# Kernel tuning notes

Hardware: AMD Instinct MI355X
Metric: run time of the kernel (lower is better)

The kernel has to match this reference:

```python
import jax, jax.numpy as jnp
import numpy as np

B, N, C, H = 4, 2048, 1024, 16
HD = C // H  # head dim = 64


def setup_inputs() -> dict:
    key = jax.random.key(0)
    k1, k2, k3, k4 = jax.random.split(key, 4)
    x = jax.random.normal(k1, (B, N, C), dtype=jnp.float32)
    # nn.Linear(C, 3C, bias=False): weight [3C, C], y = x @ W.T
    w_qkv = jax.random.normal(k2, (3 * C, C), dtype=jnp.float32) * (C ** -0.5)
    # nn.Linear(C, C) with bias
    w_out = jax.random.normal(k3, (C, C), dtype=jnp.float32) * (C ** -0.5)
    b_out = jax.random.normal(k4, (C,), dtype=jnp.float32) * 0.01
    return {"x": x, "w_qkv": w_qkv, "w_out": w_out, "b_out": b_out}


def reference(x, w_qkv, w_out, b_out):
    scale = HD ** -0.5
    qkv = jnp.einsum('bnc,dc->bnd', x, w_qkv)  # [B, N, 3C]
    q, k, v = jnp.split(qkv, 3, axis=-1)
    # rearrange 'b n (h c) -> b h n c'
    def heads(t):
        return t.reshape(B, N, H, HD).transpose(0, 2, 1, 3)
    q, k, v = heads(q) * scale, heads(k), heads(v)
    scores = jnp.einsum('bhnc,bhmc->bhnm', q, k)  # [B, H, N, N]
    attn = jax.nn.softmax(scores, axis=-1)
    v_hat = jnp.einsum('bhnm,bhmc->bhnc', attn, v)
    out = v_hat.transpose(0, 2, 1, 3).reshape(B, N, C)  # 'b h n c -> b n (h c)'
    return jnp.einsum('bnc,dc->bnd', out, w_out) + b_out
```

## Files before the change

kernel.cpp:

```cpp
#include <hip/hip_runtime.h>

typedef unsigned short ushort_t;
typedef __attribute__((ext_vector_type(8))) short short8;
typedef __attribute__((ext_vector_type(4))) float f32x4;
typedef __attribute__((ext_vector_type(16))) float f32x16;
typedef __attribute__((ext_vector_type(4))) float float4v;
typedef __attribute__((ext_vector_type(4))) unsigned short ushortx4;
typedef __attribute__((ext_vector_type(4))) unsigned int uint4v;

#define AS1 __attribute__((address_space(1)))
#define AS3 __attribute__((address_space(3)))

#define B_ 4
#define N_ 2048
#define C_ 1024
#define H_ 16
#define HD_ 64
#define M_TOT 8192
#define N3_ 3072

#define QSCALE 0.18033688011112042f

__device__ __forceinline__ unsigned short f2bf(float f) {
    unsigned int u = __float_as_uint(f);
    u += 0x7fffu + ((u >> 16) & 1u);
    return (unsigned short)(u >> 16);
}

__global__ __launch_bounds__(256) void cast_f32_bf16(const float* __restrict__ in,
                                                     ushort_t* __restrict__ out, int n4) {
    int i = blockIdx.x * blockDim.x + threadIdx.x;
    int stride = gridDim.x * blockDim.x;
    for (; i < n4; i += stride) {
        float4v v = ((const float4v*)in)[i];
        ushortx4 o;
        o[0] = f2bf(v[0]); o[1] = f2bf(v[1]); o[2] = f2bf(v[2]); o[3] = f2bf(v[3]);
        ((ushortx4*)out)[i] = o;
    }
}


template <int EPI>
__global__ __launch_bounds__(256) void gemm_bt(const ushort_t* __restrict__ A,
                                               const ushort_t* __restrict__ Bw,
                                               ushort_t* __restrict__ o0,
                                               ushort_t* __restrict__ o1,
                                               ushort_t* __restrict__ o2,
                                               float* __restrict__ outf,
                                               const float* __restrict__ bias, int K) {
    __shared__ ushort_t As[2][128 * 32];
    __shared__ ushort_t Bs[2][128 * 32];
    const int tid = threadIdx.x;
    const int lane = tid & 63;
    const int wid = tid >> 6;
    const int l15 = lane & 15, lg = lane >> 4;
    const int wr = wid >> 1, wc = wid & 1;
    const int m0 = blockIdx.y * 128, n0 = blockIdx.x * 128;

    f32x4 acc[4][4] = {};

    auto stage = [&](int buf, int k0) {
        int row = tid >> 2;
        int ko = (tid & 3) * 8;
        const ushort_t* a0 = A + (size_t)(m0 + row) * K + k0 + ko;
        const ushort_t* b0 = Bw + (size_t)(n0 + row) * K + k0 + ko;
        char* la = (char*)(&As[buf][0]) + (tid & 192) * 16;
        char* lb = (char*)(&Bs[buf][0]) + (tid & 192) * 16;
        __builtin_amdgcn_global_load_lds((const AS1 void*)a0, (AS3 void*)la, 16, 0, 0);
        __builtin_amdgcn_global_load_lds((const AS1 void*)(a0 + (size_t)64 * K),
                                         (AS3 void*)(la + 4096), 16, 0, 0);
        __builtin_amdgcn_global_load_lds((const AS1 void*)b0, (AS3 void*)lb, 16, 0, 0);
        __builtin_amdgcn_global_load_lds((const AS1 void*)(b0 + (size_t)64 * K),
                                         (AS3 void*)(lb + 4096), 16, 0, 0);
    };

    stage(0, 0);
    __syncthreads();
    const int NKI = K >> 5;
    for (int kt = 0; kt < NKI; ++kt) {
        const int cur = kt & 1;
        if (kt + 1 < NKI) stage(cur ^ 1, (kt + 1) << 5);
        short8 af[4], bf[4];
#pragma unroll
        for (int mi = 0; mi < 4; ++mi)
            af[mi] = *(const short8*)(&As[cur][(wr * 64 + mi * 16 + l15) * 32 + lg * 8]);
#pragma unroll
        for (int ni = 0; ni < 4; ++ni)
            bf[ni] = *(const short8*)(&Bs[cur][(wc * 64 + ni * 16 + l15) * 32 + lg * 8]);
#pragma unroll
        for (int mi = 0; mi < 4; ++mi)
#pragma unroll
            for (int ni = 0; ni < 4; ++ni)
                acc[mi][ni] = __builtin_amdgcn_mfma_f32_16x16x32_bf16(af[mi], bf[ni],
                                                                      acc[mi][ni], 0, 0, 0);
        __syncthreads();
    }

    if (EPI == 0) {
        const int sel = blockIdx.x >> 3;
        const int cb = (blockIdx.x & 7) * 128 + wc * 64;
#pragma unroll
        for (int mi = 0; mi < 4; ++mi) {
            const int r0 = m0 + wr * 64 + mi * 16 + lg * 4;
            const int b = r0 >> 11, n = r0 & 2047;
            const int blk = n >> 5, nlo = n & 31;
#pragma unroll
            for (int ni = 0; ni < 4; ++ni) {
                const int c = cb + ni * 16 + l15;
                const int h = c >> 6, hd = c & 63;
                const int bh = b * H_ + h;
                f32x4 a = acc[mi][ni];
                if (sel == 2) {
                    size_t base = (((size_t)(bh * 64 + blk) * 2 + (hd >> 5)) * 2 +
                                   ((n >> 4) & 1)) * 512 +
                                  ((hd & 31) + ((n >> 3) & 1) * 32) * 8 + (n & 7);
                    ushortx4 pk;
#pragma unroll
                    for (int j = 0; j < 4; ++j) pk[j] = f2bf(a[j]);
                    *(ushortx4*)(&o2[base]) = pk;
                } else {
                    size_t base = ((size_t)(bh * 64 + blk) * 4 + (hd >> 4)) * 512 +
                                  (nlo + ((hd >> 3) & 1) * 32) * 8 + (hd & 7);
                    if (sel == 0) {
#pragma unroll
                        for (int j = 0; j < 4; ++j) o0[base + j * 8] = f2bf(a[j] * QSCALE);
                    } else {
#pragma unroll
                        for (int j = 0; j < 4; ++j) o1[base + j * 8] = f2bf(a[j]);
                    }
                }
            }
        }
    } else {
#pragma unroll
        for (int ni = 0; ni < 4; ++ni) {
            const int c = n0 + wc * 64 + ni * 16 + l15;
            const float bv = bias[c];
#pragma unroll
            for (int mi = 0; mi < 4; ++mi) {
                const int r0 = m0 + wr * 64 + mi * 16 + lg * 4;
                f32x4 a = acc[mi][ni];
#pragma unroll
                for (int j = 0; j < 4; ++j)
                    outf[(size_t)(r0 + j) * C_ + c] = a[j] + bv;
            }
        }
    }
}

__global__ __launch_bounds__(256, 2) void attn_fwd(const ushort_t* __restrict__ Qf,
                                                   const ushort_t* __restrict__ Kf,
                                                   const ushort_t* __restrict__ Vf,
                                                   ushort_t* __restrict__ Ov) {
    const int tid = threadIdx.x;
    const int lane = tid & 63;
    const int wid = tid >> 6;
    const int lc = lane & 31, lh = lane >> 5;

    const int wg = blockIdx.x;
    const int xcd = wg & 7, slot = wg >> 3;
    const int bh = xcd * 8 + (slot >> 3);
    const int qt = slot & 7;

    const ushort_t* qpb = Qf + (size_t)bh * N_ * HD_;
    const ushort_t* kpb = Kf + (size_t)bh * N_ * HD_;
    const ushort_t* vpb = Vf + (size_t)bh * N_ * HD_;

    const int qblk0 = qt * 8 + wid * 2;

    short8 qf[2][4];
#pragma unroll
    for (int qc = 0; qc < 2; ++qc)
#pragma unroll
        for (int ks = 0; ks < 4; ++ks)
            qf[qc][ks] = *(const short8*)(qpb + ((size_t)(qblk0 + qc) * 4 + ks) * 512 +
                                          lane * 8);

    {
        const int ph = (wid + (wg & 3)) & 3;
        if (ph == 1) __builtin_amdgcn_s_sleep(3);
        else if (ph == 2) __builtin_amdgcn_s_sleep(6);
        else if (ph == 3) __builtin_amdgcn_s_sleep(9);
    }

    f32x16 oacc[2][2] = {};
    float srun[2] = {0.f, 0.f};

    short8 kfA[4], kfB[4], vfA[4], vfB[4];
#pragma unroll
    for (int ks = 0; ks < 4; ++ks)
        kfA[ks] = *(const short8*)(kpb + (size_t)ks * 512 + lane * 8);
#pragma unroll
    for (int dt = 0; dt < 2; ++dt)
#pragma unroll
        for (int kb = 0; kb < 2; ++kb)
            vfA[dt * 2 + kb] = *(const short8*)(vpb + ((size_t)dt * 2 + kb) * 512 + lane * 8);

    auto iter = [&](short8(&kfu)[4], short8(&kfp)[4], short8(&vfu)[4], short8(&vfp)[4],
                    int t) {
        f32x16 sacc[2] = {};
        __builtin_amdgcn_s_setprio(1);
#pragma unroll
        for (int ks = 0; ks < 4; ++ks)
#pragma unroll
            for (int qc = 0; qc < 2; ++qc)
                sacc[qc] = __builtin_amdgcn_mfma_f32_32x32x16_bf16(kfu[ks], qf[qc][ks],
                                                                   sacc[qc], 0, 0, 0);
        __builtin_amdgcn_s_setprio(0);

        const int kvn = (t + 1) & 63;
#pragma unroll
        for (int ks = 0; ks < 4; ++ks)
            kfp[ks] = *(const short8*)(kpb + ((size_t)kvn * 4 + ks) * 512 + lane * 8);
#pragma unroll
        for (int dt = 0; dt < 2; ++dt)
#pragma unroll
            for (int kb = 0; kb < 2; ++kb)
                vfp[dt * 2 + kb] = *(const short8*)(vpb + (((size_t)kvn * 2 + dt) * 2 + kb) *
                                                    512 + lane * 8);

#pragma unroll
        for (int qc = 0; qc < 2; ++qc) {
            float p[16];
#pragma unroll
            for (int r = 0; r < 16; ++r) p[r] = __builtin_amdgcn_exp2f(sacc[qc][r]);
            float s01 = (p[0] + p[1]) + (p[2] + p[3]);
            float s23 = (p[4] + p[5]) + (p[6] + p[7]);
            float s45 = (p[8] + p[9]) + (p[10] + p[11]);
            float s67 = (p[12] + p[13]) + (p[14] + p[15]);
            srun[qc] += (s01 + s23) + (s45 + s67);

            unsigned pk[4][2];
#pragma unroll
            for (int r1 = 0; r1 < 4; ++r1)
#pragma unroll
                for (int c = 0; c < 2; ++c)
                    asm("v_cvt_pk_bf16_f32 %0, %1, %2"
                        : "=v"(pk[r1][c])
                        : "v"(p[4 * r1 + 2 * c]), "v"(p[4 * r1 + 2 * c + 1]));

            short8 pb[2];
#pragma unroll
            for (int kb = 0; kb < 2; ++kb) {
                unsigned a0 = pk[2 * kb][0], b0 = pk[2 * kb + 1][0];
                unsigned a1 = pk[2 * kb][1], b1 = pk[2 * kb + 1][1];
                asm("v_permlane32_swap_b32 %0, %1" : "+v"(a0), "+v"(b0));
                asm("v_permlane32_swap_b32 %0, %1" : "+v"(a1), "+v"(b1));
                uint4v w;
                w[0] = a0; w[1] = a1; w[2] = b0; w[3] = b1;
                pb[kb] = __builtin_bit_cast(short8, w);
            }

            __builtin_amdgcn_s_setprio(1);
#pragma unroll
            for (int dt = 0; dt < 2; ++dt)
#pragma unroll
                for (int kb = 0; kb < 2; ++kb)
                    oacc[qc][dt] = __builtin_amdgcn_mfma_f32_32x32x16_bf16(
                        vfu[dt * 2 + kb], pb[kb], oacc[qc][dt], 0, 0, 0);
            __builtin_amdgcn_s_setprio(0);
        }
    };

    for (int t2 = 0; t2 < 64; t2 += 2) {
        iter(kfA, kfB, vfA, vfB, t2);
        iter(kfB, kfA, vfB, vfA, t2 + 1);
    }

    const int b = bh >> 4, h = bh & 15;
#pragma unroll
    for (int qc = 0; qc < 2; ++qc) {
        float s = srun[qc];
        s += __shfl_xor(s, 32, 64);
        const float inv = 1.f / s;
        const int qg = (qblk0 + qc) * 32 + lc;
        ushort_t* orow = Ov + (size_t)(b * N_ + qg) * C_ + h * HD_;
#pragma unroll
        for (int dt = 0; dt < 2; ++dt)
#pragma unroll
            for (int r1 = 0; r1 < 4; ++r1) {
                ushortx4 pkv;
#pragma unroll
                for (int r0 = 0; r0 < 4; ++r0)
                    pkv[r0] = f2bf(oacc[qc][dt][4 * r1 + r0] * inv);
                *(ushortx4*)(orow + dt * 32 + r1 * 8 + lh * 4) = pkv;
            }
    }
}

extern "C" void kernel_launch(void* const* d_in, const int* in_sizes, int n_in,
                              void* d_out, int out_size, void* d_ws, size_t ws_size,
                              hipStream_t stream) {
    const float* x = (const float*)d_in[0];
    const float* wqkv = (const float*)d_in[1];
    const float* wout = (const float*)d_in[2];
    const float* bout = (const float*)d_in[3];
    float* out = (float*)d_out;

    ushort_t* ws = (ushort_t*)d_ws;
    const size_t XN = (size_t)M_TOT * C_;
    const size_t WQN = (size_t)N3_ * C_;
    const size_t WON = (size_t)C_ * C_;
    ushort_t* xbf = ws;
    ushort_t* wqkvb = xbf + XN;
    ushort_t* woutb = wqkvb + WQN;
    ushort_t* karr = woutb + WON;
    ushort_t* varr = karr + XN;
    ushort_t* qarr = varr + XN;
    ushort_t* vhat = xbf;

    cast_f32_bf16<<<2048, 256, 0, stream>>>(x, xbf, (int)(XN / 4));
    cast_f32_bf16<<<1024, 256, 0, stream>>>(wqkv, wqkvb, (int)(WQN / 4));
    cast_f32_bf16<<<512, 256, 0, stream>>>(wout, woutb, (int)(WON / 4));

    gemm_bt<0><<<dim3(24, 64), 256, 0, stream>>>(xbf, wqkvb, qarr, karr, varr,
                                                 nullptr, nullptr, C_);
    attn_fwd<<<512, 256, 0, stream>>>(qarr, karr, varr, vhat);
    gemm_bt<1><<<dim3(8, 64), 256, 0, stream>>>(vhat, woutb, nullptr, nullptr, nullptr,
                                                out, bout, C_);
}
```

Baseline: 194.0 us.

## Rewrite projection GEMMs with 256x128 tiles, swizzled LDS and explicit pipelining

```diff
diff --git a/kernel.cpp b/kernel.cpp
--- a/kernel.cpp
+++ b/kernel.cpp
@@ -39,66 +39,96 @@
     }
 }
 
-
 template <int EPI>
-__global__ __launch_bounds__(256) void gemm_bt(const ushort_t* __restrict__ A,
-                                               const ushort_t* __restrict__ Bw,
-                                               ushort_t* __restrict__ o0,
-                                               ushort_t* __restrict__ o1,
-                                               ushort_t* __restrict__ o2,
-                                               float* __restrict__ outf,
-                                               const float* __restrict__ bias, int K) {
-    __shared__ ushort_t As[2][128 * 32];
-    __shared__ ushort_t Bs[2][128 * 32];
+__global__ __launch_bounds__(512, 2) void gemm8p(const ushort_t* __restrict__ A,
+                                                 const ushort_t* __restrict__ Bw,
+                                                 ushort_t* __restrict__ o0,
+                                                 ushort_t* __restrict__ o1,
+                                                 ushort_t* __restrict__ o2,
+                                                 float* __restrict__ outf,
+                                                 const float* __restrict__ bias,
+                                                 int K, int NBX) {
+    extern __shared__ ushort_t smem[];
     const int tid = threadIdx.x;
     const int lane = tid & 63;
     const int wid = tid >> 6;
     const int l15 = lane & 15, lg = lane >> 4;
-    const int wr = wid >> 1, wc = wid & 1;
-    const int m0 = blockIdx.y * 128, n0 = blockIdx.x * 128;
+    const int wr = wid >> 1;
+    const int wc = wid & 1;
+
+    const int wg = blockIdx.x;
+    const int id = (wg & 7) * ((int)gridDim.x >> 3) + (wg >> 3);
+    const int by = id / NBX, bx = id - by * NBX;
+    const int m0 = by * 256, n0 = bx * 128;
+
+    const int koff = (((lane >> 4) ^ ((lane >> 1) & 3)) << 3);
+    const int trow = tid >> 2;
+    const int slotsrc = (tid & 3) ^ ((tid >> 3) & 3);
+
+    auto stageA = [&](int q, int tt, int kh, int c) {
+        const ushort_t* src = A + (size_t)(m0 + c * 128 + trow) * K + tt * 64 + kh * 32 +
+                              slotsrc * 8;
+        ushort_t* dst = smem + q * 24576 + kh * 8192 + c * 4096 + tid * 8;
+        __builtin_amdgcn_global_load_lds((const AS1 void*)src, (AS3 void*)dst, 16, 0, 0);
+    };
+    auto stageB = [&](int q, int tt, int kh) {
+        const ushort_t* src = Bw + (size_t)(n0 + trow) * K + tt * 64 + kh * 32 + slotsrc * 8;
+        ushort_t* dst = smem + q * 24576 + 16384 + kh * 4096 + tid * 8;
+        __builtin_amdgcn_global_load_lds((const AS1 void*)src, (AS3 void*)dst, 16, 0, 0);
+    };
 
     f32x4 acc[4][4] = {};
 
-    auto stage = [&](int buf, int k0) {
-        int row = tid >> 2;
-        int ko = (tid & 3) * 8;
-        const ushort_t* a0 = A + (size_t)(m0 + row) * K + k0 + ko;
-        const ushort_t* b0 = Bw + (size_t)(n0 + row) * K + k0 + ko;
-        char* la = (char*)(&As[buf][0]) + (tid & 192) * 16;
-        char* lb = (char*)(&Bs[buf][0]) + (tid & 192) * 16;
-        __builtin_amdgcn_global_load_lds((const AS1 void*)a0, (AS3 void*)la, 16, 0, 0);
-        __builtin_amdgcn_global_load_lds((const AS1 void*)(a0 + (size_t)64 * K),
-                                         (AS3 void*)(la + 4096), 16, 0, 0);
-        __builtin_amdgcn_global_load_lds((const AS1 void*)b0, (AS3 void*)lb, 16, 0, 0);
-        __builtin_amdgcn_global_load_lds((const AS1 void*)(b0 + (size_t)64 * K),
-                                         (AS3 void*)(lb + 4096), 16, 0, 0);
+    auto phase = [&](int p, int kh) {
+        const ushort_t* Ab = smem + p * 24576 + kh * 8192;
+        const ushort_t* Bb = smem + p * 24576 + 16384 + kh * 4096;
+        short8 af[4], bfr[4];
+#pragma unroll
+        for (int rt = 0; rt < 4; ++rt)
+            af[rt] = *(const short8*)(Ab + (wr * 64 + rt * 16 + l15) * 32 + koff);
+#pragma unroll
+        for (int ni = 0; ni < 4; ++ni)
+            bfr[ni] = *(const short8*)(Bb + (wc * 64 + ni * 16 + l15) * 32 + koff);
+        __builtin_amdgcn_s_setprio(1);
+#pragma unroll
+        for (int rt = 0; rt < 4; ++rt)
+#pragma unroll
+            for (int ni = 0; ni < 4; ++ni)
+                acc[rt][ni] = __builtin_amdgcn_mfma_f32_16x16x32_bf16(af[rt], bfr[ni],
+                                                                      acc[rt][ni], 0, 0, 0);
+        __builtin_amdgcn_s_setprio(0);
     };
 
-    stage(0, 0);
-    __syncthreads();
-    const int NKI = K >> 5;
-    for (int kt = 0; kt < NKI; ++kt) {
-        const int cur = kt & 1;
-        if (kt + 1 < NKI) stage(cur ^ 1, (kt + 1) << 5);
-        short8 af[4], bf[4];
-#pragma unroll
-        for (int mi = 0; mi < 4; ++mi)
-            af[mi] = *(const short8*)(&As[cur][(wr * 64 + mi * 16 + l15) * 32 + lg * 8]);
-#pragma unroll
-        for (int ni = 0; ni < 4; ++ni)
-            bf[ni] = *(const short8*)(&Bs[cur][(wc * 64 + ni * 16 + l15) * 32 + lg * 8]);
-#pragma unroll
-        for (int mi = 0; mi < 4; ++mi)
-#pragma unroll
-            for (int ni = 0; ni < 4; ++ni)
-                acc[mi][ni] = __builtin_amdgcn_mfma_f32_16x16x32_bf16(af[mi], bf[ni],
-                                                                      acc[mi][ni], 0, 0, 0);
-        __syncthreads();
+    stageA(0, 0, 0, 0); stageA(0, 0, 0, 1);
+    stageA(0, 0, 1, 0); stageA(0, 0, 1, 1);
+    stageB(0, 0, 0);    stageB(0, 0, 1);
+
+    const int NT = K >> 6;
+    for (int t = 0; t < NT; ++t) {
+        const int p = t & 1, q = p ^ 1;
+        if (t + 1 < NT) {
+            stageA(q, t + 1, 0, 0); stageA(q, t + 1, 0, 1);
+            __builtin_amdgcn_sched_barrier(0);
+            asm volatile("s_waitcnt vmcnt(2)");
+        } else {
+            asm volatile("s_waitcnt vmcnt(0)");
+        }
+        __builtin_amdgcn_sched_barrier(0);
+        __builtin_amdgcn_s_barrier();
+        __builtin_amdgcn_sched_barrier(0);
+        phase(p, 0);
+        if (t + 1 < NT) {
+            stageA(q, t + 1, 1, 0); stageA(q, t + 1, 1, 1);
+            stageB(q, t + 1, 0);    stageB(q, t + 1, 1);
+        }
+        __builtin_amdgcn_sched_barrier(0);
+        __builtin_amdgcn_s_barrier();
+        __builtin_amdgcn_sched_barrier(0);
+        phase(p, 1);
     }
 
     if (EPI == 0) {
-        const int sel = blockIdx.x >> 3;
-        const int cb = (blockIdx.x & 7) * 128 + wc * 64;
+        const int sel = bx >> 3;
 #pragma unroll
         for (int mi = 0; mi < 4; ++mi) {
             const int r0 = m0 + wr * 64 + mi * 16 + lg * 4;
@@ -106,8 +136,8 @@
             const int blk = n >> 5, nlo = n & 31;
 #pragma unroll
             for (int ni = 0; ni < 4; ++ni) {
-                const int c = cb + ni * 16 + l15;
-                const int h = c >> 6, hd = c & 63;
+                const int cq = (bx & 7) * 128 + wc * 64 + ni * 16 + l15;
+                const int h = cq >> 6, hd = cq & 63;
                 const int bh = b * H_ + h;
                 f32x4 a = acc[mi][ni];
                 if (sel == 2) {
@@ -175,13 +205,6 @@
         for (int ks = 0; ks < 4; ++ks)
             qf[qc][ks] = *(const short8*)(qpb + ((size_t)(qblk0 + qc) * 4 + ks) * 512 +
                                           lane * 8);
-
-    {
-        const int ph = (wid + (wg & 3)) & 3;
-        if (ph == 1) __builtin_amdgcn_s_sleep(3);
-        else if (ph == 2) __builtin_amdgcn_s_sleep(6);
-        else if (ph == 3) __builtin_amdgcn_s_sleep(9);
-    }
 
     f32x16 oacc[2][2] = {};
     float srun[2] = {0.f, 0.f};
@@ -313,9 +336,9 @@
     cast_f32_bf16<<<1024, 256, 0, stream>>>(wqkv, wqkvb, (int)(WQN / 4));
     cast_f32_bf16<<<512, 256, 0, stream>>>(wout, woutb, (int)(WON / 4));
 
-    gemm_bt<0><<<dim3(24, 64), 256, 0, stream>>>(xbf, wqkvb, qarr, karr, varr,
-                                                 nullptr, nullptr, C_);
+    gemm8p<0><<<768, 512, 98304, stream>>>(xbf, wqkvb, qarr, karr, varr,
+                                           nullptr, nullptr, C_, 24);
     attn_fwd<<<512, 256, 0, stream>>>(qarr, karr, varr, vhat);
-    gemm_bt<1><<<dim3(8, 64), 256, 0, stream>>>(vhat, woutb, nullptr, nullptr, nullptr,
-                                                out, bout, C_);
-}
+    gemm8p<1><<<256, 512, 98304, stream>>>(vhat, woutb, nullptr, nullptr, nullptr,
+                                           out, bout, C_, 8);
+}
```

Result: faster. 180.1 us (-7.2%).
